# Kernel tuning notes

Measured on AMD Instinct MI355X. Metric: run time of the kernel, lower is better.

Reference implementation:

```python
import jax, jax.numpy as jnp
import numpy as np
from jax import lax


def affine_grid(theta, H, W):
    # theta [2,3]; torch F.affine_grid, align_corners=False (pixel centers)
    xs = (jnp.arange(W, dtype=jnp.float32) * 2 + 1) / W - 1
    ys = (jnp.arange(H, dtype=jnp.float32) * 2 + 1) / H - 1
    gx, gy = jnp.meshgrid(xs, ys)  # [H,W]
    base = jnp.stack([gx, gy, jnp.ones_like(gx)], -1)  # [H,W,3]
    return jnp.einsum('hwk,jk->hwj', base, theta)  # [H,W,2]


def grid_sample(img, grid):
    # img [C,H,W], grid [H,W,2] normalized; bilinear, zero padding, align_corners=False
    C, H, W = img.shape
    x = ((grid[..., 0] + 1) * W - 1) * 0.5
    y = ((grid[..., 1] + 1) * H - 1) * 0.5
    x0 = jnp.floor(x); y0 = jnp.floor(y)
    x1 = x0 + 1; y1 = y0 + 1
    wx1 = x - x0; wx0 = 1 - wx1
    wy1 = y - y0; wy0 = 1 - wy1
    def gather(xi, yi):
        xic = jnp.clip(xi, 0, W - 1).astype(jnp.int32)
        yic = jnp.clip(yi, 0, H - 1).astype(jnp.int32)
        valid = ((xi >= 0) & (xi <= W - 1) & (yi >= 0) & (yi <= H - 1)).astype(img.dtype)
        return img[:, yic, xic] * valid  # [C,H,W]
    return (gather(x0, y0) * (wx0 * wy0) + gather(x1, y0) * (wx1 * wy0)
            + gather(x0, y1) * (wx0 * wy1) + gather(x1, y1) * (wx1 * wy1))


def warp_one(feat, t):
    # feat [C,H,W], t [4,4]: rotate then translate, two bilinear resamples (as in source)
    C, H, W = feat.shape
    zero = jnp.zeros((), feat.dtype); one = jnp.ones((), feat.dtype)
    theta_rot = jnp.stack([jnp.stack([t[0, 0], t[0, 1], zero]),
                           jnp.stack([t[1, 0], t[1, 1], zero])])
    x_tr = 4 * t[0, 3] / 128
    y_tr = -(4 * t[1, 3]) / 128
    theta_tr = jnp.stack([jnp.stack([one, zero, x_tr]),
                          jnp.stack([zero, one, y_tr])])
    f = grid_sample(feat, affine_grid(theta_rot, H, W))
    return grid_sample(f, affine_grid(theta_tr, H, W))


def conv2d(x, w, b):
    y = lax.conv_general_dilated(x, w, (1, 1), 'SAME',
                                 dimension_numbers=('NCHW', 'OIHW', 'NCHW'))
    return y + b[None, :, None, None]


def convgru_step0(x, wx, wh, bx, bh):
    # single-layer ConvGRU, one timestep, h0 = 0 => hidden convs vanish, only bh remains
    C = wh.shape[1]
    gx = conv2d(x, wx, bx)  # [N,3C,H,W]
    xr, xz, xn = jnp.split(gx, 3, axis=1)
    br, bz, bn = jnp.split(bh, 3)
    r = jax.nn.sigmoid(xr + br[None, :, None, None])
    z = jax.nn.sigmoid(xz + bz[None, :, None, None])
    n = jnp.tanh(xn + r * bn[None, :, None, None])
    return (1 - z) * n  # h' = (1-z)*n + z*0


def setup_inputs() -> dict:
    key = jax.random.key(0)
    ks = jax.random.split(key, 6)
    B, A, C, H, W = 2, 5, 64, 128, 128
    feats = jax.random.normal(ks[0], (B, A, C, H, W), jnp.float32)
    ang = jax.random.uniform(ks[1], (B, A, A), minval=-np.pi, maxval=np.pi).astype(jnp.float32)
    ca, sa = jnp.cos(ang), jnp.sin(ang)
    t = jnp.zeros((B, A, A, 4, 4), jnp.float32)
    t = t.at[..., 0, 0].set(ca).at[..., 0, 1].set(-sa)
    t = t.at[..., 1, 0].set(sa).at[..., 1, 1].set(ca)
    tr = jax.random.uniform(ks[2], (B, A, A, 2), minval=-10.0, maxval=10.0)
    t = t.at[..., 0, 3].set(tr[..., 0]).at[..., 1, 3].set(tr[..., 1])
    wx = jax.random.normal(ks[3], (3 * C, 2 * C, 3, 3), jnp.float32) * 0.05
    wh = jax.random.normal(ks[4], (3 * C, C, 3, 3), jnp.float32) * 0.05
    bx = jnp.zeros((3 * C,), jnp.float32)
    bh = jnp.zeros((3 * C,), jnp.float32)
    return {'feats': feats, 'trans': t, 'wx': wx, 'wh': wh, 'bx': bx, 'bh': bh,
            'num_agent': A, 'gnn_iter': 2}


def reference(feats, trans, wx, wh, bx, bh, num_agent, gnn_iter):
    trans = lax.stop_gradient(trans)  # source builds theta via torch.tensor (detached)
    B, A, C, H, W = feats.shape
    mask = 1.0 - jnp.eye(A, dtype=feats.dtype)  # exclude self (j != i)
    warp = jax.vmap(jax.vmap(jax.vmap(warp_one, (0, 0)), (None, 0)), (0, 0))
    for _ in range(gnn_iter):
        warped = warp(feats, trans)  # [B, A_i, A_j, C, H, W]
        mean = jnp.einsum('bijchw,ij->bichw', warped, mask) / (A - 1)
        cat = jnp.concatenate([feats, mean], axis=2).reshape(B * A, 2 * C, H, W)
        feats = convgru_step0(cat, wx, wh, bx, bh).reshape(B, A, C, H, W)
    return feats
```

## Files before the change

kernel.cpp:

```cpp
#include <hip/hip_runtime.h>
#include <cmath>

#define BB 2
#define AA 5
#define CH 64
#define HH 128
#define WW 128
#define HW (HH*WW)
#define NIMG (BB*AA)

typedef __attribute__((ext_vector_type(8))) _Float16 half8;
typedef __attribute__((ext_vector_type(2))) _Float16 half2v;
typedef __attribute__((ext_vector_type(4))) float floatx4;
typedef unsigned int uint32;
typedef __attribute__((ext_vector_type(4))) uint32 uint4v;

__device__ inline half8 hzero() {
    half8 v;
#pragma unroll
    for (int e = 0; e < 8; ++e) v[e] = (_Float16)0.f;
    return v;
}

__device__ inline float fsigmoid(float x) {
    return __builtin_amdgcn_rcpf(1.f + __builtin_amdgcn_exp2f(-1.442695041f * x));
}
__device__ inline float ftanh(float x) {
    return 2.f * fsigmoid(2.f * x) - 1.f;
}

__global__ __launch_bounds__(256) void to_nhwc_kernel(
    const float* __restrict__ src, _Float16* __restrict__ dst)
{
    const int img = blockIdx.y;
    const int cg  = blockIdx.x & 7;
    const int pb  = blockIdx.x >> 3;
    const int p   = pb * 256 + threadIdx.x;
    const float* s = src + ((size_t)img * CH + cg * 8) * HW + p;
    half8 v;
#pragma unroll
    for (int e = 0; e < 8; ++e) v[e] = (_Float16)s[e * HW];
    *(half8*)(dst + ((size_t)img * HW + p) * 128 + cg * 8) = v;
}

__global__ __launch_bounds__(256) void pack_w_kernel(
    const float* __restrict__ wx, half8* __restrict__ wp)
{
    int idx = blockIdx.x * 256 + threadIdx.x;
    if (idx >= 4 * 9 * 4 * 192) return;
    int oc = idx % 192; int r = idx / 192;
    int gk = r & 3; r >>= 2; int tap = r % 9; int cc = r / 9;
    int ky = tap / 3, kx = tap % 3;
    half8 v;
#pragma unroll
    for (int e = 0; e < 8; ++e)
        v[e] = (_Float16)wx[(((size_t)oc * 128 + cc * 32 + gk * 8 + e) * 3 + ky) * 3 + kx];
    wp[idx] = v;
}

__global__ __launch_bounds__(256, 5) void warp_mean_kernel(
    const _Float16* __restrict__ nh,
    const float* __restrict__ trans,
    _Float16* __restrict__ nhw)
{
    __shared__ uint32 f_lds[32 * 9 * 18];

    const int tile = blockIdx.x;
    const int tx0 = (tile & 7) * 16;
    const int ty0 = (tile >> 3) * 8;
    const int bi  = blockIdx.z;
    const int b   = bi / AA, i = bi % AA;
    const int tid = threadIdx.x;

    const int slc = tid & 7;
    const int ptb = tid >> 3;
    const int col = tid & 15;
    const int row = (tid >> 4) & 7;
    const int chh = tid >> 7;

    half2v acc[16];
#pragma unroll
    for (int c = 0; c < 16; ++c) acc[c] = (half2v)(_Float16)0.f;

    for (int j = 0; j < AA; ++j) {
        if (j == i) continue;
        const float* t = trans + (((size_t)b * AA + i) * AA + j) * 16;
        const float t00 = t[0], t01 = t[1], t03 = t[3];
        const float t10 = t[4], t11 = t[5], t13 = t[7];
        const float dxs = 2.f * t03;
        const float dys = -2.f * t13;
        const float sxf = floorf(dxs), syf = floorf(dys);
        const int sx = (int)sxf, sy = (int)syf;
        const float fx = dxs - sxf, fy = dys - syf;
        const _Float16* srcj = nh + (size_t)(b * AA + j) * HW * 128 + slc * 8;

        __syncthreads();
#pragma unroll
        for (int it = 0; it < 5; ++it) {
            const int pt = it * 32 + ptb;
            if (pt < 153) {
                const int prow = pt / 17;
                const int pcol = pt - prow * 17;
                const int qx = tx0 + sx + pcol;
                const int qy = ty0 + sy + prow;
                float e[8];
#pragma unroll
                for (int k = 0; k < 8; ++k) e[k] = 0.f;
                if (((unsigned)qx < (unsigned)WW) & ((unsigned)qy < (unsigned)HH)) {
                    const float xn = (2 * qx + 1) * (1.0f / WW) - 1.f;
                    const float yn = (2 * qy + 1) * (1.0f / HH) - 1.f;
                    const float px = 64.f * (t00 * xn + t01 * yn) + 63.5f;
                    const float py = 64.f * (t10 * xn + t11 * yn) + 63.5f;
                    const float x0f = floorf(px), y0f = floorf(py);
                    const int x0 = (int)x0f, y0 = (int)y0f;
                    const float wx1 = px - x0f, wx0 = 1.f - wx1;
                    const float wy1 = py - y0f, wy0 = 1.f - wy1;
                    const bool vx0 = (x0 >= 0) & (x0 < WW);
                    const bool vx1 = (x0 + 1 >= 0) & (x0 + 1 < WW);
                    const bool vy0 = (y0 >= 0) & (y0 < HH);
                    const bool vy1 = (y0 + 1 >= 0) & (y0 + 1 < HH);
                    const int cx0 = min(max(x0, 0), WW - 1);
                    const int cx1 = min(max(x0 + 1, 0), WW - 1);
                    const int cy0 = min(max(y0, 0), HH - 1);
                    const int cy1 = min(max(y0 + 1, 0), HH - 1);
                    const float w00 = (vx0 & vy0) ? wx0 * wy0 : 0.f;
                    const float w01 = (vx1 & vy0) ? wx1 * wy0 : 0.f;
                    const float w10 = (vx0 & vy1) ? wx0 * wy1 : 0.f;
                    const float w11 = (vx1 & vy1) ? wx1 * wy1 : 0.f;
                    const half8 A = *(const half8*)(srcj + ((size_t)cy0 * WW + cx0) * 128);
                    const half8 Bv = *(const half8*)(srcj + ((size_t)cy0 * WW + cx1) * 128);
                    const half8 Cv = *(const half8*)(srcj + ((size_t)cy1 * WW + cx0) * 128);
                    const half8 D = *(const half8*)(srcj + ((size_t)cy1 * WW + cx1) * 128);
#pragma unroll
                    for (int k = 0; k < 8; ++k)
                        e[k] = w00 * (float)A[k] + w01 * (float)Bv[k]
                             + w10 * (float)Cv[k] + w11 * (float)D[k];
                }
                const int lb = slc * 4 * 162 + prow * 18 + pcol;
#pragma unroll
                for (int k = 0; k < 4; ++k) {
                    half2v p;
                    p[0] = (_Float16)e[2 * k];
                    p[1] = (_Float16)e[2 * k + 1];
                    f_lds[lb + k * 162] = __builtin_bit_cast(uint32, p);
                }
            }
        }
        __syncthreads();

        const float wAf = (1.f - fx) * (1.f - fy);
        const float wBf = fx * (1.f - fy);
        const float wCf = (1.f - fx) * fy;
        const float wDf = fx * fy;
        half2v wA2 = (half2v)(_Float16)wAf;
        half2v wB2 = (half2v)(_Float16)wBf;
        half2v wC2 = (half2v)(_Float16)wCf;
        half2v wD2 = (half2v)(_Float16)wDf;
        const uint32* fp0 = f_lds + (chh * 16) * 162 + row * 18 + col;
#pragma unroll
        for (int c = 0; c < 16; ++c) {
            const uint32* fp = fp0 + c * 162;
            const half2v v00 = __builtin_bit_cast(half2v, fp[0]);
            const half2v v01 = __builtin_bit_cast(half2v, fp[1]);
            const half2v v10 = __builtin_bit_cast(half2v, fp[18]);
            const half2v v11 = __builtin_bit_cast(half2v, fp[19]);
            acc[c] += v00 * wA2 + v01 * wB2 + v10 * wC2 + v11 * wD2;
        }
    }

    const half2v q = (half2v)(_Float16)0.25f;
    uint32 os[16];
#pragma unroll
    for (int c = 0; c < 16; ++c) os[c] = __builtin_bit_cast(uint32, acc[c] * q);
    uint4v* dst = (uint4v*)(nhw + ((size_t)bi * HW + (ty0 + row) * WW + tx0 + col) * 128
                            + 64 + chh * 32);
#pragma unroll
    for (int k = 0; k < 4; ++k)
        dst[k] = (uint4v){os[4 * k], os[4 * k + 1], os[4 * k + 2], os[4 * k + 3]};
}

__global__ __launch_bounds__(256, 4) void conv_gru_mfma(
    const _Float16* __restrict__ in,
    const half8* __restrict__ wp,
    const float* __restrict__ bx,
    const float* __restrict__ bh,
    float* __restrict__ out_f32,
    _Float16* __restrict__ out_f16)
{
    __shared__ half8 lds_in[16 * 6 * 18];

    const int tid = threadIdx.x;
    const int img = blockIdx.z;
    const int x0 = (blockIdx.x & 7) * 16;
    const int y0 = (blockIdx.x >> 3) * 4;
    const int w   = tid >> 6;
    const int ln  = tid & 15;
    const int kq  = (tid & 63) >> 4;

    const _Float16* inimg = in + (size_t)img * HW * 128;
    for (int f = tid; f < 1728; f += 256) {
        const int g = f / 108; const int r = f % 108;
        const int row = r / 18; const int col = r % 18;
        const int y = y0 + row - 1, x = x0 + col - 1;
        half8 v = hzero();
        if ((unsigned)x < (unsigned)WW && (unsigned)y < (unsigned)HH)
            v = *(const half8*)(inimg + ((size_t)y * WW + x) * 128 + g * 8);
        lds_in[f] = v;
    }

    floatx4 acc[4][3];
#pragma unroll
    for (int s = 0; s < 4; ++s)
#pragma unroll
        for (int t = 0; t < 3; ++t)
#pragma unroll
            for (int r = 0; r < 4; ++r) acc[s][t][r] = 0.f;

    __syncthreads();

    const half8* wbase = wp + kq * 192 + w * 16 + ln;
    half8 bp0[3], bp1[3];
#pragma unroll
    for (int t = 0; t < 3; ++t) bp0[t] = wbase[t * 64];
#pragma unroll
    for (int t = 0; t < 3; ++t) bp1[t] = wbase[768 + t * 64];

#pragma unroll
    for (int s = 0; s < 36; ++s) {
        const int cc = s / 9, tap = s - cc * 9;
        const int dy = tap / 3, dx = tap - dy * 3;
        half8 bcur[3];
#pragma unroll
        for (int t = 0; t < 3; ++t) { bcur[t] = bp0[t]; bp0[t] = bp1[t]; }
        if (s + 2 < 36) {
            const half8* wsrc = wbase + (size_t)(s + 2) * 768;
#pragma unroll
            for (int t = 0; t < 3; ++t) bp1[t] = wsrc[t * 64];
        }
        half8 a[4];
#pragma unroll
        for (int t = 0; t < 4; ++t)
            a[t] = lds_in[((cc * 4 + kq) * 6 + t + dy) * 18 + ln + dx];
#pragma unroll
        for (int t = 0; t < 4; ++t)
#pragma unroll
            for (int u = 0; u < 3; ++u)
                acc[t][u] = __builtin_amdgcn_mfma_f32_16x16x32_f16(a[t], bcur[u], acc[t][u], 0, 0, 0);
    }

    const int c = w * 16 + ln;
    const float bxr = bx[c] + bh[c];
    const float bxz = bx[64 + c] + bh[64 + c];
    const float bxn = bx[128 + c];
    const float bnn = bh[128 + c];
#pragma unroll
    for (int s = 0; s < 4; ++s) {
        const int y = y0 + s;
#pragma unroll
        for (int reg = 0; reg < 4; ++reg) {
            const int x = x0 + kq * 4 + reg;
            const float xr = acc[s][0][reg] + bxr;
            const float xz = acc[s][1][reg] + bxz;
            const float xn = acc[s][2][reg] + bxn;
            const float rg = fsigmoid(xr);
            const float zg = fsigmoid(xz);
            const float n  = ftanh(xn + rg * bnn);
            const float h  = (1.f - zg) * n;
            if (out_f32)
                out_f32[((size_t)img * CH + c) * HW + y * WW + x] = h;
            else
                out_f16[((size_t)img * HW + y * WW + x) * 128 + c] = (_Float16)h;
        }
    }
}

extern "C" void kernel_launch(void* const* d_in, const int* in_sizes, int n_in,
                              void* d_out, int out_size, void* d_ws, size_t ws_size,
                              hipStream_t stream) {
    const float* feats = (const float*)d_in[0];
    const float* trans = (const float*)d_in[1];
    const float* wx    = (const float*)d_in[2];
    const float* bx    = (const float*)d_in[4];
    const float* bh    = (const float*)d_in[5];
    float* out = (float*)d_out;

    char* ws = (char*)d_ws;
    half8*    wpack = (half8*)ws;
    _Float16* B1 = (_Float16*)(ws + 442368);
    _Float16* B2 = (_Float16*)(ws + 442368 + (size_t)NIMG * HW * 128 * 2);

    pack_w_kernel<<<108, 256, 0, stream>>>(wx, wpack);
    to_nhwc_kernel<<<dim3(512, NIMG), 256, 0, stream>>>(feats, B1);

    dim3 wgrid(128, 1, NIMG);
    dim3 cgrid(256, 1, NIMG);

    warp_mean_kernel<<<wgrid, 256, 0, stream>>>(B1, trans, B1);
    conv_gru_mfma<<<cgrid, 256, 0, stream>>>(B1, wpack, bx, bh, nullptr, B2);
    warp_mean_kernel<<<wgrid, 256, 0, stream>>>(B2, trans, B2);
    conv_gru_mfma<<<cgrid, 256, 0, stream>>>(B2, wpack, bx, bh, out, nullptr);
}
```

Before: 332.7 us.

## Software-pipeline LDS A-fragment reads with inline asm and padded LDS layout

Replaces the unrolled K loop in the ConvGRU MFMA kernel with a template-recursive loop that issues ds_read_b128 for the next step's A fragments via inline asm, then waits with an explicit lgkmcnt before running the current step's MFMAs. This overlaps LDS latency with matrix math. The LDS tile is padded to 110 entries per channel group, likely to cut bank conflicts and allow immediate offsets. Launch bounds drop from 4 to 3 waves per SIMD to make room for the extra registers, which trades occupancy for the double-buffered fragments.

```diff
diff --git a/kernel.cpp b/kernel.cpp
--- a/kernel.cpp
+++ b/kernel.cpp
@@ -179,7 +179,56 @@
         dst[k] = (uint4v){os[4 * k], os[4 * k + 1], os[4 * k + 2], os[4 * k + 3]};
 }
 
-__global__ __launch_bounds__(256, 4) void conv_gru_mfma(
+#define APL 110
+
+template <int S>
+__device__ __forceinline__ void issue_a(uint32 abase, half8 (&dst)[4]) {
+    constexpr int cc = S / 9, tap = S % 9, dy = tap / 3, dx = tap % 3;
+    constexpr int base = ((cc * 4) * APL + dy * 18 + dx) * 16;
+    asm volatile("ds_read_b128 %0, %1 offset:%c2"
+                 : "=&v"(dst[0]) : "v"(abase), "i"(base + 0 * 288));
+    asm volatile("ds_read_b128 %0, %1 offset:%c2"
+                 : "=&v"(dst[1]) : "v"(abase), "i"(base + 1 * 288));
+    asm volatile("ds_read_b128 %0, %1 offset:%c2"
+                 : "=&v"(dst[2]) : "v"(abase), "i"(base + 2 * 288));
+    asm volatile("ds_read_b128 %0, %1 offset:%c2"
+                 : "=&v"(dst[3]) : "v"(abase), "i"(base + 3 * 288));
+}
+
+template <int S>
+struct KLoop {
+    static __device__ __forceinline__ void run(
+        const half8* __restrict__ wbase, uint32 abase,
+        half8 (&cur)[4], half8 (&nxt)[4],
+        half8 (&bp0)[3], half8 (&bp1)[3], floatx4 (&acc)[4][3])
+    {
+        if constexpr (S + 1 < 36) issue_a<(S + 1 < 36) ? S + 1 : 0>(abase, nxt);
+        asm volatile("s_waitcnt lgkmcnt(%c0)" :: "i"((S + 1 < 36) ? 4 : 0) : "memory");
+        __builtin_amdgcn_sched_barrier(0);
+        half8 bcur[3];
+#pragma unroll
+        for (int t = 0; t < 3; ++t) { bcur[t] = bp0[t]; bp0[t] = bp1[t]; }
+        if constexpr (S + 2 < 36) {
+            const half8* wsrc = wbase + (size_t)(S + 2) * 768;
+#pragma unroll
+            for (int t = 0; t < 3; ++t) bp1[t] = wsrc[t * 64];
+        }
+#pragma unroll
+        for (int t = 0; t < 4; ++t)
+#pragma unroll
+            for (int u = 0; u < 3; ++u)
+                acc[t][u] = __builtin_amdgcn_mfma_f32_16x16x32_f16(cur[t], bcur[u], acc[t][u], 0, 0, 0);
+        KLoop<S + 1>::run(wbase, abase, nxt, cur, bp0, bp1, acc);
+    }
+};
+template <>
+struct KLoop<36> {
+    static __device__ __forceinline__ void run(
+        const half8* __restrict__, uint32, half8 (&)[4], half8 (&)[4],
+        half8 (&)[3], half8 (&)[3], floatx4 (&)[4][3]) {}
+};
+
+__global__ __launch_bounds__(256, 3) void conv_gru_mfma(
     const _Float16* __restrict__ in,
     const half8* __restrict__ wp,
     const float* __restrict__ bx,
@@ -187,7 +236,7 @@
     float* __restrict__ out_f32,
     _Float16* __restrict__ out_f16)
 {
-    __shared__ half8 lds_in[16 * 6 * 18];
+    __shared__ half8 lds_in[16 * APL];
 
     const int tid = threadIdx.x;
     const int img = blockIdx.z;
@@ -205,7 +254,7 @@
         half8 v = hzero();
         if ((unsigned)x < (unsigned)WW && (unsigned)y < (unsigned)HH)
             v = *(const half8*)(inimg + ((size_t)y * WW + x) * 128 + g * 8);
-        lds_in[f] = v;
+        lds_in[g * APL + r] = v;
     }
 
     floatx4 acc[4][3];
@@ -225,28 +274,11 @@
 #pragma unroll
     for (int t = 0; t < 3; ++t) bp1[t] = wbase[768 + t * 64];
 
-#pragma unroll
-    for (int s = 0; s < 36; ++s) {
-        const int cc = s / 9, tap = s - cc * 9;
-        const int dy = tap / 3, dx = tap - dy * 3;
-        half8 bcur[3];
-#pragma unroll
-        for (int t = 0; t < 3; ++t) { bcur[t] = bp0[t]; bp0[t] = bp1[t]; }
-        if (s + 2 < 36) {
-            const half8* wsrc = wbase + (size_t)(s + 2) * 768;
-#pragma unroll
-            for (int t = 0; t < 3; ++t) bp1[t] = wsrc[t * 64];
-        }
-        half8 a[4];
-#pragma unroll
-        for (int t = 0; t < 4; ++t)
-            a[t] = lds_in[((cc * 4 + kq) * 6 + t + dy) * 18 + ln + dx];
-#pragma unroll
-        for (int t = 0; t < 4; ++t)
-#pragma unroll
-            for (int u = 0; u < 3; ++u)
-                acc[t][u] = __builtin_amdgcn_mfma_f32_16x16x32_f16(a[t], bcur[u], acc[t][u], 0, 0, 0);
-    }
+    const uint32 abase = (uint32)(size_t)(&lds_in[0]) + (uint32)((kq * APL + ln) * 16);
+
+    half8 aA[4], aB[4];
+    issue_a<0>(abase, aA);
+    KLoop<0>::run(wbase, abase, aA, aB, bp0, bp1, acc);
 
     const int c = w * 16 + ln;
     const float bxr = bx[c] + bh[c];
```

After: 343.6 us. 3.3% more time.
